# Optimization experiments

Measured on AMD Instinct MI355X. Metric: run time of the kernel, lower is better.

Reference implementation:

```python
import jax, jax.numpy as jnp
import numpy as np

B, N, IN_DIM, HID, OUT_DIM, CODEBOOK = 32, 2048, 128, 64, 64, 2048


def setup_inputs() -> dict:
    key = jax.random.key(0)
    ks = jax.random.split(key, 6)
    # xavier-uniform-ish scales for the MLP weights
    def xavier(k, fan_in, fan_out):
        gain = float(np.sqrt(2.0))  # relu gain
        lim = gain * np.sqrt(6.0 / (fan_in + fan_out))
        return jax.random.uniform(k, (fan_in, fan_out), jnp.float32, -lim, lim)
    return {
        "obs": jax.random.normal(ks[0], (B, N, IN_DIM), jnp.float32),
        "W1": xavier(ks[1], IN_DIM, HID),
        "b1": jnp.full((HID,), 0.01, jnp.float32),
        "W2": xavier(ks[2], HID, HID),
        "b2": jnp.full((HID,), 0.01, jnp.float32),
        "W3": xavier(ks[3], HID, OUT_DIM),
        "b3": jnp.full((OUT_DIM,), 0.01, jnp.float32),
        "codebook": jax.random.normal(ks[4], (CODEBOOK, OUT_DIM), jnp.float32),
    }


def reference(obs, W1, b1, W2, b2, W3, b3, codebook):
    # --- tiny MLP ---
    h = jax.nn.relu(obs @ W1 + b1)
    h = jax.nn.relu(h @ W2 + b2)
    x = h @ W3 + b3  # [B, N, D]

    # --- vector quantize: euclidean nearest codebook entry ---
    x2 = jnp.sum(x * x, axis=-1, keepdims=True)           # [B, N, 1]
    e2 = jnp.sum(codebook * codebook, axis=-1)            # [C]
    dist = x2 - 2.0 * jnp.einsum("bnd,cd->bnc", x, codebook) + e2  # [B, N, C]
    idx = jnp.argmin(dist, axis=-1)                        # [B, N] int
    quantize = codebook[idx]                               # [B, N, D] gather

    # commitment loss: mse(sg(quantize), x)
    cmt_loss = jnp.mean((jax.lax.stop_gradient(quantize) - x) ** 2)
    # straight-through estimator
    msg = x + jax.lax.stop_gradient(quantize - x)
    return (msg, idx, cmt_loss)
```

## Files before the change

### kernel.cpp

```cpp
#include <hip/hip_runtime.h>


#define NPTS    65536
#define IN_DIM  128
#define HID     64
#define OUT_DIM 64
#define CB_N    2048
#define MSG_ELEMS (NPTS * OUT_DIM)
#define LOSS_SCALE (1.0f / 4194304.0f)
#define MARG 0.5f
#define CAND_CAP 1024
#define BPTS 128
#define NTHR 512

typedef __attribute__((ext_vector_type(8))) short short8;
typedef _Float16 half8 __attribute__((ext_vector_type(8)));
typedef __attribute__((ext_vector_type(4))) float f32x4;
typedef unsigned int u32;
typedef unsigned long long u64;

__device__ __forceinline__ void gld16(void* lds_base, const void* gsrc) {
    __builtin_amdgcn_global_load_lds(
        (const __attribute__((address_space(1))) u32*)gsrc,
        (__attribute__((address_space(3))) u32*)lds_base, 16, 0, 0);
}

__global__ __launch_bounds__(256) void prep_all(
    const float* __restrict__ cb,
    const float* __restrict__ W1, const float* __restrict__ W2,
    const float* __restrict__ W3,
    float* __restrict__ e2,
    _Float16* __restrict__ cbh,
    _Float16* __restrict__ w1h, _Float16* __restrict__ w1l,
    _Float16* __restrict__ w2h, _Float16* __restrict__ w2l,
    _Float16* __restrict__ w3h, _Float16* __restrict__ w3l,
    float* __restrict__ loss)
{
    const int b = blockIdx.x, tid = threadIdx.x;
    if (b < 64) {
        const int id = b * 256 + tid;
        const int n = id >> 3, h = (id >> 2) & 1, quad = id & 3;
        const int t = n >> 4, l15 = n & 15;
        const float* src = cb + (long)n * OUT_DIM + h * 32 + quad * 8;
        half8 hi;
        #pragma unroll
        for (int j = 0; j < 8; ++j)
            hi[j] = (_Float16)src[j];
        const long dst = ((long)(t * 2 + h) * 64 + quad * 16 + l15) * 8;
        *(half8*)(cbh + dst) = hi;
    } else if (b < 72) {
        const int id = (b - 64) * 256 + tid;
        const int lane = id & 63;
        const int m = lane & 15, quad = lane >> 4;
        const float* W; _Float16 *dh, *dl; int frag;
        if (id < 1024)      { W = W1; dh = w1h; dl = w1l; frag = id >> 6; }
        else if (id < 1536) { W = W2; dh = w2h; dl = w2l; frag = (id - 1024) >> 6; }
        else                { W = W3; dh = w3h; dl = w3l; frag = (id - 1536) >> 6; }
        const int kc = frag >> 2, nt = frag & 3;
        half8 hi, lo;
        #pragma unroll
        for (int j = 0; j < 8; ++j) {
            const float v = W[(long)(kc * 32 + quad * 8 + j) * 64 + nt * 16 + m];
            hi[j] = (_Float16)v;
            lo[j] = (_Float16)(v - (float)hi[j]);
        }
        const long dst = (long)(frag * 64 + lane) * 8;
        *(half8*)(dh + dst) = hi;
        *(half8*)(dl + dst) = lo;
    } else {
        if (b == 72 && tid == 0) *loss = 0.0f;
        const int c = (b - 72) * 256 + tid;
        const float4* row = (const float4*)(cb + (long)c * OUT_DIM);
        float s = 0.0f;
        #pragma unroll
        for (int mq = 0; mq < 16; ++mq) {
            const float4 v = row[mq];
            s += v.x * v.x + v.y * v.y + v.z * v.z + v.w * v.w;
        }
        e2[c] = s;
    }
}

#define MFMA16(A, B, C) __builtin_amdgcn_mfma_f32_16x16x32_f16(A, B, C, 0, 0, 0)

__device__ __forceinline__ void split16(const float* xs, half8& h, half8& l) {
    #pragma unroll
    for (int j = 0; j < 8; ++j) {
        h[j] = (_Float16)xs[j];
        l[j] = (_Float16)(xs[j] - (float)h[j]);
    }
}

__device__ __forceinline__ u64 packkey(float d, int n) {
    u32 ub = __float_as_uint(d);
    ub = (ub & 0x80000000u) ? ~ub : (ub | 0x80000000u);
    return ((u64)ub << 32) | (u32)n;
}

__device__ __forceinline__ float exdist(
    const float* __restrict__ xr, const float* __restrict__ cbrow, float e2v)
{
    const float4* xp = (const float4*)xr;
    const float4* cp = (const float4*)cbrow;
    float a0 = 0.0f, a1 = 0.0f;
    #pragma unroll
    for (int mq = 0; mq < 16; ++mq) {
        const float4 xv = xp[mq], cv = cp[mq];
        a0 = fmaf(xv.x, cv.x, a0); a1 = fmaf(xv.y, cv.y, a1);
        a0 = fmaf(xv.z, cv.z, a0); a1 = fmaf(xv.w, cv.w, a1);
    }
    return fmaf(-2.0f, a0 + a1, e2v);
}

__global__ __launch_bounds__(NTHR, 4) void fused_mlp_vq(
    const float* __restrict__ obs,
    const float* __restrict__ b1, const float* __restrict__ b2,
    const float* __restrict__ b3,
    const _Float16* __restrict__ w1h, const _Float16* __restrict__ w1l,
    const _Float16* __restrict__ w2h, const _Float16* __restrict__ w2l,
    const _Float16* __restrict__ w3h, const _Float16* __restrict__ w3l,
    const float* __restrict__ cb,
    const _Float16* __restrict__ cbhp,
    const float* __restrict__ e2,
    float* __restrict__ msg,
    float* __restrict__ idx_out,
    float* __restrict__ loss_out)
{
    __shared__ __align__(16) char smem[65536];
    __shared__ float e2s[CB_N];
    __shared__ int   cand_pc[CAND_CAP];
    __shared__ u64   keys[BPTS];
    __shared__ int   win_sh[BPTS];
    __shared__ int   idx_sh[BPTS];
    __shared__ float wred[NTHR / 64];
    __shared__ int   cand_cnt;

    const int t = threadIdx.x, lane = t & 63, w = t >> 6;
    const int m = lane & 15, quad = lane >> 4;
    const long base = (long)blockIdx.x * BPTS;
    float* hbuf = (float*)smem;
    const int row0 = w * 16 + quad * 4;
    const int arow_l = w * 16 + m;

    if (t == 0) cand_cnt = 0;
    if (t < BPTS) keys[t] = ~0ULL;
    ((float4*)e2s)[t] = ((const float4*)e2)[t];

    {
        float bb1[4], bb2[4], bb3[4];
        #pragma unroll
        for (int nt = 0; nt < 4; ++nt) {
            bb1[nt] = b1[nt * 16 + m];
            bb2[nt] = b2[nt * 16 + m];
            bb3[nt] = b3[nt * 16 + m];
        }

        const float* arow = obs + (base + w * 16 + m) * IN_DIM;
        half8 a1h[4], a1l[4];
        #pragma unroll
        for (int kc = 0; kc < 4; ++kc) {
            const float4 va = *(const float4*)(arow + kc * 32 + quad * 8);
            const float4 vb = *(const float4*)(arow + kc * 32 + quad * 8 + 4);
            const float xs[8] = {va.x, va.y, va.z, va.w, vb.x, vb.y, vb.z, vb.w};
            split16(xs, a1h[kc], a1l[kc]);
        }

        #pragma unroll
        for (int nt = 0; nt < 4; ++nt) {
            f32x4 acc = {0.0f, 0.0f, 0.0f, 0.0f};
            #pragma unroll
            for (int kc = 0; kc < 4; ++kc) {
                const long fo = (long)((kc * 4 + nt) * 64 + lane) * 8;
                const half8 wh = *(const half8*)(w1h + fo);
                const half8 wl = *(const half8*)(w1l + fo);
                acc = MFMA16(a1h[kc], wh, acc);
                acc = MFMA16(a1l[kc], wh, acc);
                acc = MFMA16(a1h[kc], wl, acc);
            }
            #pragma unroll
            for (int r = 0; r < 4; ++r) {
                const float v = acc[r] + bb1[nt];
                hbuf[(row0 + r) * 68 + nt * 16 + m] = v > 0.0f ? v : 0.0f;
            }
        }

        half8 a2h[2], a2l[2];
        #pragma unroll
        for (int kc = 0; kc < 2; ++kc) {
            const float4 va = *(const float4*)&hbuf[arow_l * 68 + kc * 32 + quad * 8];
            const float4 vb = *(const float4*)&hbuf[arow_l * 68 + kc * 32 + quad * 8 + 4];
            const float xs[8] = {va.x, va.y, va.z, va.w, vb.x, vb.y, vb.z, vb.w};
            split16(xs, a2h[kc], a2l[kc]);
        }
        #pragma unroll
        for (int nt = 0; nt < 4; ++nt) {
            f32x4 acc = {0.0f, 0.0f, 0.0f, 0.0f};
            #pragma unroll
            for (int kc = 0; kc < 2; ++kc) {
                const long fo = (long)((kc * 4 + nt) * 64 + lane) * 8;
                const half8 wh = *(const half8*)(w2h + fo);
                const half8 wl = *(const half8*)(w2l + fo);
                acc = MFMA16(a2h[kc], wh, acc);
                acc = MFMA16(a2l[kc], wh, acc);
                acc = MFMA16(a2h[kc], wl, acc);
            }
            #pragma unroll
            for (int r = 0; r < 4; ++r) {
                const float v = acc[r] + bb2[nt];
                hbuf[(row0 + r) * 68 + nt * 16 + m] = v > 0.0f ? v : 0.0f;
            }
        }

        half8 a3h[2], a3l[2];
        #pragma unroll
        for (int kc = 0; kc < 2; ++kc) {
            const float4 va = *(const float4*)&hbuf[arow_l * 68 + kc * 32 + quad * 8];
            const float4 vb = *(const float4*)&hbuf[arow_l * 68 + kc * 32 + quad * 8 + 4];
            const float xs[8] = {va.x, va.y, va.z, va.w, vb.x, vb.y, vb.z, vb.w};
            split16(xs, a3h[kc], a3l[kc]);
        }
        #pragma unroll
        for (int nt = 0; nt < 4; ++nt) {
            f32x4 acc = {0.0f, 0.0f, 0.0f, 0.0f};
            #pragma unroll
            for (int kc = 0; kc < 2; ++kc) {
                const long fo = (long)((kc * 4 + nt) * 64 + lane) * 8;
                const half8 wh = *(const half8*)(w3h + fo);
                const half8 wl = *(const half8*)(w3l + fo);
                acc = MFMA16(a3h[kc], wh, acc);
                acc = MFMA16(a3l[kc], wh, acc);
                acc = MFMA16(a3h[kc], wl, acc);
            }
            #pragma unroll
            for (int r = 0; r < 4; ++r)
                hbuf[(row0 + r) * 68 + nt * 16 + m] = acc[r] + bb3[nt];
        }
    }

    half8 a0h, a1h;
    {
        const float* xrow = &hbuf[(w * 16 + m) * 68];
        const float4 xa = *(const float4*)(xrow + quad * 8);
        const float4 xb = *(const float4*)(xrow + quad * 8 + 4);
        const float4 xc = *(const float4*)(xrow + 32 + quad * 8);
        const float4 xd = *(const float4*)(xrow + 32 + quad * 8 + 4);
        const float x0[8] = {xa.x, xa.y, xa.z, xa.w, xb.x, xb.y, xb.z, xb.w};
        const float x1[8] = {xc.x, xc.y, xc.z, xc.w, xd.x, xd.y, xd.z, xd.w};
        #pragma unroll
        for (int j = 0; j < 8; ++j) {
            a0h[j] = (_Float16)x0[j];
            a1h[j] = (_Float16)x1[j];
        }
    }
    __syncthreads();

    {
        float4* mg = (float4*)(msg + base * OUT_DIM);
        #pragma unroll
        for (int mm = 0; mm < 4; ++mm) {
            const int v = t + NTHR * mm;
            const int p = v >> 4, k4 = v & 15;
            mg[v] = *(const float4*)&hbuf[p * 68 + k4 * 4];
        }
    }
    __syncthreads();

    float bd[4] = {3.4e38f, 3.4e38f, 3.4e38f, 3.4e38f};
    int   bi[4] = {0, 0, 0, 0};

    for (int qp = 0; qp < 4; ++qp) {
        const _Float16* cbq = cbhp + (long)qp * 32768;
        #pragma unroll
        for (int j = 0; j < 8; ++j)
            gld16(smem + j * 8192 + w * 1024, cbq + j * 4096 + w * 512 + lane * 8);
        __syncthreads();

        #pragma unroll 4
        for (int tl = 0; tl < 32; ++tl) {
            const int g = qp * 32 + tl;
            const half8 th0 = *(const half8*)(smem + tl * 2048 + lane * 16);
            const half8 th1 = *(const half8*)(smem + tl * 2048 + 1024 + lane * 16);
            const float e2v = e2s[g * 16 + m];
            f32x4 acc = {0.0f, 0.0f, 0.0f, 0.0f};
            __builtin_amdgcn_s_setprio(1);
            acc = MFMA16(a0h, th0, acc);
            acc = MFMA16(a1h, th1, acc);
            __builtin_amdgcn_s_setprio(0);

            const int code = g * 16 + m;
            bool pushm[4]; int pip[4];
            #pragma unroll
            for (int r = 0; r < 4; ++r) {
                const float d = fmaf(-2.0f, acc[r], e2v);
                const bool lt = d < bd[r];
                pushm[r] = __builtin_fabsf(d - bd[r]) < MARG;
                pip[r] = lt ? bi[r] : code;
                bd[r] = lt ? d : bd[r];
                bi[r] = lt ? code : bi[r];
            }
            if (__any((int)(pushm[0] | pushm[1] | pushm[2] | pushm[3]))) {
                #pragma unroll
                for (int r = 0; r < 4; ++r) {
                    if (pushm[r]) {
                        const int slot = atomicAdd(&cand_cnt, 1);
                        if (slot < CAND_CAP)
                            cand_pc[slot] = ((w * 16 + quad * 4 + r) << 16) | pip[r];
                    }
                }
            }
        }
        __syncthreads();
    }

    {
        float rd[4]; int ri[4];
        #pragma unroll
        for (int r = 0; r < 4; ++r) { rd[r] = bd[r]; ri[r] = bi[r]; }
        #pragma unroll
        for (int off = 1; off <= 8; off <<= 1) {
            #pragma unroll
            for (int r = 0; r < 4; ++r) {
                const float od = __shfl_xor(rd[r], off, 64);
                const int   oi = __shfl_xor(ri[r], off, 64);
                if (od < rd[r] || (od == rd[r] && oi < ri[r])) {
                    rd[r] = od; ri[r] = oi;
                }
            }
        }
        #pragma unroll
        for (int r = 0; r < 4; ++r) {
            const int pl = w * 16 + quad * 4 + r;
            if (m == 0) win_sh[pl] = ri[r];
            if (bd[r] <= rd[r] + MARG && bi[r] != ri[r]) {
                const int slot = atomicAdd(&cand_cnt, 1);
                if (slot < CAND_CAP)
                    cand_pc[slot] = (pl << 16) | bi[r];
            }
        }
    }
    __syncthreads();

    {
        if (t < BPTS) {
            const int n = win_sh[t];
            const float ex = exdist(msg + (base + t) * OUT_DIM,
                                    cb + (long)n * OUT_DIM, e2s[n]);
            atomicMin(&keys[t], packkey(ex, n));
        }
        const int L = min(cand_cnt, CAND_CAP);
        for (int l = t; l < L; l += NTHR) {
            const int pc = cand_pc[l];
            const int p = pc >> 16, n = pc & 0xFFFF;
            const float ex = exdist(msg + (base + p) * OUT_DIM,
                                    cb + (long)n * OUT_DIM, e2s[n]);
            atomicMin(&keys[p], packkey(ex, n));
        }
    }
    __syncthreads();

    if (t < BPTS) {
        const int code = (int)(keys[t] & 0xFFFFFFFFu);
        idx_sh[t] = code;
        idx_out[base + t] = (float)code;
    }
    __syncthreads();

    float lsum = 0.0f;
    float4* mg = (float4*)(msg + base * OUT_DIM);
    #pragma unroll
    for (int mm = 0; mm < 4; ++mm) {
        const int v = t + NTHR * mm;
        const int p = v >> 4, k4 = v & 15;
        const int code = idx_sh[p];
        const float4 q = ((const float4*)(cb + (long)code * OUT_DIM))[k4];
        const float4 xv = mg[v];
        const float dx = q.x - xv.x, dy = q.y - xv.y;
        const float dz = q.z - xv.z, dw2 = q.w - xv.w;
        lsum += dx * dx + dy * dy + dz * dz + dw2 * dw2;
        mg[v] = q;
    }
    #pragma unroll
    for (int off = 32; off > 0; off >>= 1) lsum += __shfl_down(lsum, off, 64);
    if (lane == 0) wred[w] = lsum;
    __syncthreads();
    if (t == 0) {
        float s = 0.0f;
        #pragma unroll
        for (int i = 0; i < NTHR / 64; ++i) s += wred[i];
        atomicAdd(loss_out, s * LOSS_SCALE);
    }
}

extern "C" void kernel_launch(void* const* d_in, const int* in_sizes, int n_in,
                              void* d_out, int out_size, void* d_ws, size_t ws_size,
                              hipStream_t stream) {
    const float* obs = (const float*)d_in[0];
    const float* W1  = (const float*)d_in[1];
    const float* b1  = (const float*)d_in[2];
    const float* W2  = (const float*)d_in[3];
    const float* b2  = (const float*)d_in[4];
    const float* W3  = (const float*)d_in[5];
    const float* b3  = (const float*)d_in[6];
    const float* cb  = (const float*)d_in[7];

    float* out  = (float*)d_out;
    float* msg  = out;
    float* idxf = out + MSG_ELEMS;
    float* loss = out + MSG_ELEMS + NPTS;

    char* ws = (char*)d_ws;
    float*     e2  = (float*)ws;
    _Float16*  cbh = (_Float16*)(ws + 8192);
    _Float16* w1h = (_Float16*)(ws + 532480);
    _Float16* w1l = (_Float16*)(ws + 548864);
    _Float16* w2h = (_Float16*)(ws + 565248);
    _Float16* w2l = (_Float16*)(ws + 573440);
    _Float16* w3h = (_Float16*)(ws + 581632);
    _Float16* w3l = (_Float16*)(ws + 589824);

    prep_all<<<80, 256, 0, stream>>>(cb, W1, W2, W3, e2, cbh,
                                     w1h, w1l, w2h, w2l, w3h, w3l, loss);
    fused_mlp_vq<<<NPTS / BPTS, NTHR, 0, stream>>>(
        obs, b1, b2, b3, w1h, w1l, w2h, w2l, w3h, w3l,
        cb, cbh, e2, msg, idxf, loss);
}
```

Baseline: 165.7 us.

## Double-buffer codebook staging and keep MLP output in LDS instead of global

```diff
diff --git a/kernel.cpp b/kernel.cpp
--- a/kernel.cpp
+++ b/kernel.cpp
@@ -98,7 +98,7 @@
 }
 
 __device__ __forceinline__ float exdist(
-    const float* __restrict__ xr, const float* __restrict__ cbrow, float e2v)
+    const float* xr, const float* __restrict__ cbrow, float e2v)
 {
     const float4* xp = (const float4*)xr;
     const float4* cp = (const float4*)cbrow;
@@ -126,8 +126,8 @@
     float* __restrict__ idx_out,
     float* __restrict__ loss_out)
 {
-    __shared__ __align__(16) char smem[65536];
-    __shared__ float e2s[CB_N];
+    __shared__ float hbuf[BPTS * 68];
+    __shared__ __align__(16) char stg[2][16384];
     __shared__ int   cand_pc[CAND_CAP];
     __shared__ u64   keys[BPTS];
     __shared__ int   win_sh[BPTS];
@@ -138,13 +138,11 @@
     const int t = threadIdx.x, lane = t & 63, w = t >> 6;
     const int m = lane & 15, quad = lane >> 4;
     const long base = (long)blockIdx.x * BPTS;
-    float* hbuf = (float*)smem;
     const int row0 = w * 16 + quad * 4;
     const int arow_l = w * 16 + m;
 
     if (t == 0) cand_cnt = 0;
     if (t < BPTS) keys[t] = ~0ULL;
-    ((float4*)e2s)[t] = ((const float4*)e2)[t];
 
     {
         float bb1[4], bb2[4], bb3[4];
@@ -252,35 +250,31 @@
             a1h[j] = (_Float16)x1[j];
         }
     }
-    __syncthreads();
-
-    {
-        float4* mg = (float4*)(msg + base * OUT_DIM);
-        #pragma unroll
-        for (int mm = 0; mm < 4; ++mm) {
-            const int v = t + NTHR * mm;
-            const int p = v >> 4, k4 = v & 15;
-            mg[v] = *(const float4*)&hbuf[p * 68 + k4 * 4];
-        }
-    }
+
+    #pragma unroll
+    for (int j = 0; j < 2; ++j)
+        gld16(stg[0] + (w * 2 + j) * 1024,
+              cbhp + (w * 2 + j) * 512 + lane * 8);
     __syncthreads();
 
     float bd[4] = {3.4e38f, 3.4e38f, 3.4e38f, 3.4e38f};
     int   bi[4] = {0, 0, 0, 0};
 
-    for (int qp = 0; qp < 4; ++qp) {
-        const _Float16* cbq = cbhp + (long)qp * 32768;
-        #pragma unroll
-        for (int j = 0; j < 8; ++j)
-            gld16(smem + j * 8192 + w * 1024, cbq + j * 4096 + w * 512 + lane * 8);
-        __syncthreads();
-
-        #pragma unroll 4
-        for (int tl = 0; tl < 32; ++tl) {
-            const int g = qp * 32 + tl;
-            const half8 th0 = *(const half8*)(smem + tl * 2048 + lane * 16);
-            const half8 th1 = *(const half8*)(smem + tl * 2048 + 1024 + lane * 16);
-            const float e2v = e2s[g * 16 + m];
+    for (int ph = 0; ph < 16; ++ph) {
+        if (ph < 15) {
+            const _Float16* cbq = cbhp + (long)(ph + 1) * 8192;
+            #pragma unroll
+            for (int j = 0; j < 2; ++j)
+                gld16(stg[(ph + 1) & 1] + (w * 2 + j) * 1024,
+                      cbq + (w * 2 + j) * 512 + lane * 8);
+        }
+        const char* bufp = stg[ph & 1];
+        #pragma unroll
+        for (int tl = 0; tl < 8; ++tl) {
+            const int g = ph * 8 + tl;
+            const half8 th0 = *(const half8*)(bufp + tl * 2048 + lane * 16);
+            const half8 th1 = *(const half8*)(bufp + tl * 2048 + 1024 + lane * 16);
+            const float e2v = e2[g * 16 + m];
             f32x4 acc = {0.0f, 0.0f, 0.0f, 0.0f};
             __builtin_amdgcn_s_setprio(1);
             acc = MFMA16(a0h, th0, acc);
@@ -343,16 +337,14 @@
     {
         if (t < BPTS) {
             const int n = win_sh[t];
-            const float ex = exdist(msg + (base + t) * OUT_DIM,
-                                    cb + (long)n * OUT_DIM, e2s[n]);
+            const float ex = exdist(&hbuf[t * 68], cb + (long)n * OUT_DIM, e2[n]);
             atomicMin(&keys[t], packkey(ex, n));
         }
         const int L = min(cand_cnt, CAND_CAP);
         for (int l = t; l < L; l += NTHR) {
             const int pc = cand_pc[l];
             const int p = pc >> 16, n = pc & 0xFFFF;
-            const float ex = exdist(msg + (base + p) * OUT_DIM,
-                                    cb + (long)n * OUT_DIM, e2s[n]);
+            const float ex = exdist(&hbuf[p * 68], cb + (long)n * OUT_DIM, e2[n]);
             atomicMin(&keys[p], packkey(ex, n));
         }
     }
@@ -373,7 +365,7 @@
         const int p = v >> 4, k4 = v & 15;
         const int code = idx_sh[p];
         const float4 q = ((const float4*)(cb + (long)code * OUT_DIM))[k4];
-        const float4 xv = mg[v];
+        const float4 xv = *(const float4*)&hbuf[p * 68 + k4 * 4];
         const float dx = q.x - xv.x, dy = q.y - xv.y;
         const float dz = q.z - xv.z, dw2 = q.w - xv.w;
         lsum += dx * dx + dy * dy + dz * dz + dw2 * dw2;
```

After: 159.6 us. -3.7%, faster.
